# Kernel optimization log

Measured on AMD Instinct MI355X. Metric: run time of the kernel, lower is better.

The kernel has to match this reference:

```python
import jax, jax.numpy as jnp
import numpy as np

B, NO, Q = 128, 36, 14          # batch, num object regions, question length
VD, QD, H = 2048, 1024, 2048    # v_dim, q_dim, FCNet hidden dim


def setup_inputs() -> dict:
    key = jax.random.key(0)
    ks = jax.random.split(key, 10)
    s = lambda fan_in: 1.0 / np.sqrt(fan_in)
    return {
        "v": jax.random.normal(ks[0], (B, NO, VD), dtype=jnp.float32),
        "q": jax.random.normal(ks[1], (B, Q, QD), dtype=jnp.float32),
        # v_net: weight_norm Linear(v_dim, 2048) + ReLU (effective weight)
        "Wv": jax.random.normal(ks[2], (H, VD), dtype=jnp.float32) * s(VD),
        "bv": jax.random.normal(ks[3], (H,), dtype=jnp.float32) * 0.01,
        # q_net: weight_norm Linear(q_dim, 2048) + ReLU
        "Wq": jax.random.normal(ks[4], (H, QD), dtype=jnp.float32) * s(QD),
        "bq": jax.random.normal(ks[5], (H,), dtype=jnp.float32) * 0.01,
        # h_net: Linear(14, 1) applied along the question axis of d_
        "wh": jax.random.normal(ks[6], (Q,), dtype=jnp.float32) * s(Q),
        "bh": jax.random.normal(ks[7], (), dtype=jnp.float32) * 0.01,
        # h_net2: Linear(v_dim, v_dim) == Linear(2048, 2048)
        "W2": jax.random.normal(ks[8], (VD, H), dtype=jnp.float32) * s(H),
        "b2": jax.random.normal(ks[9], (VD,), dtype=jnp.float32) * 0.01,
    }


def reference(v, q, Wv, bv, Wq, bq, wh, bh, W2, b2):
    # FCNet (eval mode: dropout = identity): ReLU(weight-norm Linear)
    v_ = jax.nn.relu(jnp.einsum("bnd,hd->bnh", v, Wv) + bv)  # [B, NO, H]
    q_ = jax.nn.relu(jnp.einsum("bqd,hd->bqh", q, Wq) + bq)  # [B, Q,  H]
    # Original: d_[b,h,n,q] = v_[b,n,h] * q_[b,q,h]; logits = h_net(d_)
    # => logits[b,h,n] = sum_q v_[b,n,h] * q_[b,q,h] * wh[q] + bh
    # Fused: reduce q_ against wh first, avoiding the [B,H,NO,Q] intermediate.
    qw = jnp.einsum("bqh,q->bh", q_, wh)                     # [B, H]
    logits = v_ * qw[:, None, :] + bh                        # [B, NO, H]
    # h_net2 on last dim
    return jnp.einsum("bnh,vh->bnv", logits, W2) + b2        # [B, NO, VD]
```

## Files before the change

kernel.cpp:

```cpp
#include <hip/hip_runtime.h>
#include <hip/hip_bf16.h>


typedef __attribute__((ext_vector_type(4))) float f32x4;
typedef __attribute__((ext_vector_type(8))) short short8;

__device__ __forceinline__ short f2bf(float f) {
    union { float f; unsigned u; } x; x.f = f;
    unsigned u = x.u;
    unsigned r = (u + 0x7FFFu + ((u >> 16) & 1u)) >> 16;
    return (short)(r & 0xFFFFu);
}
__device__ __forceinline__ float bf2f(short s) {
    union { unsigned u; float f; } x; x.u = ((unsigned)(unsigned short)s) << 16;
    return x.f;
}

__device__ __forceinline__ void gload_lds16(const short* g, short* l) {
    __builtin_amdgcn_global_load_lds(
        (const __attribute__((address_space(1))) unsigned int*)g,
        (__attribute__((address_space(3))) unsigned int*)l,
        16, 0, 0);
}

#define CV0 1179648
#define CV1 1703936
#define CV2 2228224
#define CV3 2457600
#define CV4 2719744
__global__ __launch_bounds__(256)
void cvt_all(const float* __restrict__ v,  short* __restrict__ vb,
             const float* __restrict__ Wv, short* __restrict__ Wvb,
             const float* __restrict__ W2, short* __restrict__ W2b,
             const float* __restrict__ q,  short* __restrict__ qb,
             const float* __restrict__ Wq, short* __restrict__ Wqb)
{
    const int stride = gridDim.x * 256;
    for (int c = blockIdx.x * 256 + threadIdx.x; c < CV4; c += stride) {
        const float* src; short* dst; int i;
        if      (c < CV0) { src = v;  dst = vb;  i = c * 8; }
        else if (c < CV1) { src = Wv; dst = Wvb; i = (c - CV0) * 8; }
        else if (c < CV2) { src = W2; dst = W2b; i = (c - CV1) * 8; }
        else if (c < CV3) { src = q;  dst = qb;  i = (c - CV2) * 8; }
        else              { src = Wq; dst = Wqb; i = (c - CV3) * 8; }
        f32x4 a = *(const f32x4*)&src[i];
        f32x4 b = *(const f32x4*)&src[i + 4];
        short8 s;
        #pragma unroll
        for (int j = 0; j < 4; ++j) { s[j] = f2bf(a[j]); s[4 + j] = f2bf(b[j]); }
        *(short8*)&dst[i] = s;
    }
}

__global__ __launch_bounds__(256)
void gemm_bt128(const short* __restrict__ Ab, const short* __restrict__ Bb,
                const float* __restrict__ bias, void* __restrict__ Cp,
                int M, int N, int K)
{
    __shared__ short ldsA[128 * 64];
    __shared__ short ldsB[128 * 64];

    const int tid    = threadIdx.x;
    const int lane   = tid & 63;
    const int wid    = tid >> 6;
    const int wr     = wid >> 1;
    const int wc     = wid & 1;
    const int lrow   = lane & 15;
    const int lchunk = lane >> 4;

    const int row0 = blockIdx.x * 128;
    const int col0 = blockIdx.y * 128;

    const int s_r = lane >> 3;
    const int s_c = ((lane & 7) ^ s_r) * 8;

    f32x4 acc[4][4];
    #pragma unroll
    for (int i = 0; i < 4; ++i)
        #pragma unroll
        for (int j = 0; j < 4; ++j)
            acc[i][j] = (f32x4)0.0f;

    const int nk = K >> 6;

    for (int kt = 0; kt < nk; ++kt) {
        const int kc = kt * 64;
        if (kt) __syncthreads();
        #pragma unroll
        for (int i = 0; i < 4; ++i) {
            const int r = wid * 32 + i * 8 + s_r;
            gload_lds16(&Ab[(size_t)(row0 + r) * K + kc + s_c],
                        &ldsA[(wid * 32 + i * 8) * 64]);
            gload_lds16(&Bb[(size_t)(col0 + r) * K + kc + s_c],
                        &ldsB[(wid * 32 + i * 8) * 64]);
        }
        __syncthreads();

        short8 af[4][2], bfv[4][2];
        #pragma unroll
        for (int mi = 0; mi < 4; ++mi) {
            const int row = wr * 64 + mi * 16 + lrow;
            #pragma unroll
            for (int ks = 0; ks < 2; ++ks)
                af[mi][ks] = *(const short8*)((const char*)ldsA +
                    row * 128 + (((ks * 4 + lchunk) * 16) ^ ((row & 7) << 4)));
        }
        #pragma unroll
        for (int ni = 0; ni < 4; ++ni) {
            const int row = wc * 64 + ni * 16 + lrow;
            #pragma unroll
            for (int ks = 0; ks < 2; ++ks)
                bfv[ni][ks] = *(const short8*)((const char*)ldsB +
                    row * 128 + (((ks * 4 + lchunk) * 16) ^ ((row & 7) << 4)));
        }
        #pragma unroll
        for (int ks = 0; ks < 2; ++ks)
            #pragma unroll
            for (int mi = 0; mi < 4; ++mi)
                #pragma unroll
                for (int ni = 0; ni < 4; ++ni)
                    acc[mi][ni] = __builtin_amdgcn_mfma_f32_16x16x32_bf16(
                        af[mi][ks], bfv[ni][ks], acc[mi][ni], 0, 0, 0);
    }

    #pragma unroll
    for (int mi = 0; mi < 4; ++mi)
        #pragma unroll
        for (int ni = 0; ni < 4; ++ni)
            #pragma unroll
            for (int r = 0; r < 4; ++r) {
                const int row = row0 + wr * 64 + mi * 16 + lchunk * 4 + r;
                const int col = col0 + wc * 64 + ni * 16 + lrow;
                float val = fmaxf(acc[mi][ni][r] + bias[col], 0.0f);
                ((short*)Cp)[(size_t)row * N + col] = f2bf(val);
            }
}

template<int EPI>
__global__ __launch_bounds__(512, 2)
void gemm256(const short* __restrict__ Ab, const short* __restrict__ Bb,
             const float* __restrict__ bias, const float* __restrict__ qw,
             const float* __restrict__ bh_p, void* __restrict__ Cp,
             int M, int N, int K)
{
    __shared__ short lds[2][4][128 * 64];

    const int tid  = threadIdx.x;
    const int lane = tid & 63;
    const int w    = tid >> 6;
    const int wr   = w >> 2;
    const int wc   = w & 3;
    const int fr   = lane & 15;
    const int fc   = lane >> 4;

    const int row0 = blockIdx.x * 256;
    const int col0 = blockIdx.y * 256;

    const int sl_s = lane >> 3;
    const int sl_c = ((lane & 7) ^ sl_s) * 8;

    const int nt = K >> 6;

    f32x4 acc[8][4];
    #pragma unroll
    for (int i = 0; i < 8; ++i)
        #pragma unroll
        for (int j = 0; j < 4; ++j)
            acc[i][j] = (f32x4)0.0f;

    auto stageA = [&](int t, int q) {
        #pragma unroll
        for (int i = 0; i < 2; ++i) {
            const int g  = w * 2 + i;
            const int rl = g * 8 + sl_s;
            const int srow = row0 + (g >> 3) * 128 + q * 64 + (rl & 63);
            gload_lds16(&Ab[(size_t)srow * K + t * 64 + sl_c],
                        &lds[t & 1][q][g * 512]);
        }
    };
    auto stageB = [&](int t, int q) {
        #pragma unroll
        for (int i = 0; i < 2; ++i) {
            const int g  = w * 2 + i;
            const int rl = g * 8 + sl_s;
            const int srow = col0 + (rl >> 5) * 64 + q * 32 + (rl & 31);
            gload_lds16(&Bb[(size_t)srow * K + t * 64 + sl_c],
                        &lds[t & 1][2 + q][g * 512]);
        }
    };

    short8 A0[4][2], A1[4][2], B0[2][2], B1[2][2];

#define READA(T, MQ, DST)                                                       \
    _Pragma("unroll") for (int m_ = 0; m_ < 4; ++m_) {                          \
        const int rl_ = wr * 64 + m_ * 16 + fr;                                 \
        _Pragma("unroll") for (int k_ = 0; k_ < 2; ++k_)                        \
            DST[m_][k_] = *(const short8*)((const char*)&lds[(T) & 1][MQ][0]    \
                + rl_ * 128 + ((k_ * 64 + fc * 16) ^ ((rl_ & 7) << 4)));        \
    }
#define READB(T, NQ, DST)                                                       \
    _Pragma("unroll") for (int n_ = 0; n_ < 2; ++n_) {                          \
        const int rl_ = wc * 32 + n_ * 16 + fr;                                 \
        _Pragma("unroll") for (int k_ = 0; k_ < 2; ++k_)                        \
            DST[n_][k_] = *(const short8*)((const char*)&lds[(T) & 1][2 + (NQ)][0] \
                + rl_ * 128 + ((k_ * 64 + fc * 16) ^ ((rl_ & 7) << 4)));        \
    }
#define MFMAQ(MQ, NQ, ASET, BSET)                                               \
    _Pragma("unroll") for (int m_ = 0; m_ < 4; ++m_)                            \
      _Pragma("unroll") for (int n_ = 0; n_ < 2; ++n_)                          \
        _Pragma("unroll") for (int k_ = 0; k_ < 2; ++k_)                        \
          acc[(MQ) * 4 + m_][(NQ) * 2 + n_] =                                   \
              __builtin_amdgcn_mfma_f32_16x16x32_bf16(                          \
                  ASET[m_][k_], BSET[n_][k_], acc[(MQ) * 4 + m_][(NQ) * 2 + n_], 0, 0, 0);

#define BAR()   asm volatile("s_barrier" ::: "memory")
#define PRIO1() __builtin_amdgcn_s_setprio(1)
#define PRIO0() __builtin_amdgcn_s_setprio(0)
#define VM4()   asm volatile("s_waitcnt vmcnt(4)" ::: "memory")
#define VM0()   asm volatile("s_waitcnt vmcnt(0)" ::: "memory")

#define KITER(T0, T1, ST1, ST2, ST3, ST4, ST5, ST6, ST7, ST8, D4, D8)           \
  {                                                                             \
          \
    READA(T0, 0, A0); READB(T0, 0, B0);                                         \
    PRIO1(); MFMAQ(0, 0, A0, B0); PRIO0();                                      \
    READB(T0, 1, B1); ST1; BAR();                                               \
                                     \
    PRIO1(); MFMAQ(0, 1, A0, B1); PRIO0();                                      \
    READA(T0, 1, A1); ST2; BAR();                                               \
                                                      \
    PRIO1(); MFMAQ(1, 1, A1, B1); PRIO0();                                      \
    ST3; BAR();                                                                 \
                                            \
    PRIO1(); MFMAQ(1, 0, A1, B0); PRIO0();                                      \
    ST4; D4; BAR();                                                             \
          \
    READA(T1, 0, A0); READB(T1, 0, B0);                                         \
    PRIO1(); MFMAQ(0, 0, A0, B0); PRIO0();                                      \
    READB(T1, 1, B1); ST5; BAR();                                               \
                                           \
    PRIO1(); MFMAQ(0, 1, A0, B1); PRIO0();                                      \
    READA(T1, 1, A1); ST6; BAR();                                               \
                                                            \
    PRIO1(); MFMAQ(1, 1, A1, B1); PRIO0();                                      \
    ST7; BAR();                                                                 \
                                                \
    PRIO1(); MFMAQ(1, 0, A1, B0); PRIO0();                                      \
    ST8; D8; BAR();                                                             \
  }

    stageA(0, 0); stageB(0, 0); stageB(0, 1); stageA(0, 1);
    stageA(1, 0); stageB(1, 1);
    VM4();
    BAR();

    const int niter = (nt >> 1) - 1;
    for (int j = 0; j < niter; ++j) {
        const int t0 = 2 * j, t1 = 2 * j + 1;
        KITER(t0, t1,
              stageA(t1, 1),     stageB(t1, 0),
              stageA(t0 + 2, 0), stageB(t0 + 2, 1),
              stageA(t0 + 2, 1), stageB(t0 + 2, 0),
              stageA(t1 + 2, 0), stageB(t1 + 2, 1),
              VM4(), VM4());
    }
    {
        const int t0 = nt - 2, t1 = nt - 1;
        KITER(t0, t1,
              stageA(t1, 1), stageB(t1, 0),
              (void)0, (void)0, (void)0, (void)0, (void)0, (void)0,
              VM0(), (void)0);
    }

#undef KITER
#undef READA
#undef READB
#undef MFMAQ
#undef BAR
#undef PRIO1
#undef PRIO0
#undef VM4
#undef VM0

    const float bhv = (EPI == 1) ? bh_p[0] : 0.0f;
    #pragma unroll
    for (int m = 0; m < 8; ++m) {
        #pragma unroll
        for (int n = 0; n < 4; ++n) {
            #pragma unroll
            for (int r = 0; r < 4; ++r) {
                const int row = row0 + wr * 128 + m * 16 + fc * 4 + r;
                const int col = col0 + wc * 64 + n * 16 + fr;
                float val = acc[m][n][r];
                if (EPI == 1) {
                    val = fmaxf(val + bias[col], 0.0f);
                    const int b = row / 36;
                    val = val * qw[b * 2048 + col] + bhv;
                    ((short*)Cp)[(size_t)row * N + col] = f2bf(val);
                } else {
                    ((float*)Cp)[(size_t)row * N + col] = val + bias[col];
                }
            }
        }
    }
}

__global__ __launch_bounds__(256)
void qw_reduce(const short* __restrict__ q_, const float* __restrict__ wh,
               float* __restrict__ qw)
{
    const int idx = blockIdx.x * 256 + threadIdx.x;
    const int b = idx >> 11;
    const int h = idx & 2047;
    float s = 0.0f;
    #pragma unroll
    for (int qq = 0; qq < 14; ++qq)
        s += bf2f(q_[(size_t)(b * 14 + qq) * 2048 + h]) * wh[qq];
    qw[idx] = s;
}

extern "C" void kernel_launch(void* const* d_in, const int* in_sizes, int n_in,
                              void* d_out, int out_size, void* d_ws, size_t ws_size,
                              hipStream_t stream)
{
    const float* v  = (const float*)d_in[0];
    const float* q  = (const float*)d_in[1];
    const float* Wv = (const float*)d_in[2];
    const float* bv = (const float*)d_in[3];
    const float* Wq = (const float*)d_in[4];
    const float* bq = (const float*)d_in[5];
    const float* wh = (const float*)d_in[6];
    const float* bh = (const float*)d_in[7];
    const float* W2 = (const float*)d_in[8];
    const float* b2 = (const float*)d_in[9];
    float* out = (float*)d_out;

    char* ws = (char*)d_ws;
    short* vb     = (short*)(ws);
    short* Wvb    = (short*)(ws + 18874368);
    short* W2b    = (short*)(ws + 27262976);
    short* qb     = (short*)(ws + 35651584);
    short* Wqb    = (short*)(ws + 39321600);
    short* q_ws   = (short*)(ws + 43515904);
    float* qw     = (float*)(ws + 50855936);
    short* logits = (short*)(ws + 51904512);

    cvt_all<<<2048, 256, 0, stream>>>(v, vb, Wv, Wvb, W2, W2b, q, qb, Wq, Wqb);

    gemm_bt128<<<dim3(1792 / 128, 2048 / 128), 256, 0, stream>>>(
        qb, Wqb, bq, q_ws, 1792, 2048, 1024);

    qw_reduce<<<(128 * 2048) / 256, 256, 0, stream>>>(q_ws, wh, qw);

    gemm256<1><<<dim3(4608 / 256, 2048 / 256), 512, 0, stream>>>(
        vb, Wvb, bv, qw, bh, logits, 4608, 2048, 2048);

    gemm256<2><<<dim3(4608 / 256, 2048 / 256), 512, 0, stream>>>(
        logits, W2b, b2, nullptr, nullptr, out, 4608, 2048, 2048);
}
```

Measured before the change: 147.5 us.

## Overlap v/Wv/W2 bf16 conversion with the q-projection GEMM in one launch

Splits the conversion kernel so only q and Wq are converted first. The v, Wv and W2 conversion now runs in extra blocks of the q-net GEMM launch (224 GEMM blocks plus 288 conversion blocks), so the memory-bound conversion overlaps the small GEMM instead of running before it. The risk is that the two kinds of work compete for bandwidth and CU slots, and the GEMM grid is now linearized with hardcoded sizes.

```diff
diff --git a/kernel.cpp b/kernel.cpp
--- a/kernel.cpp
+++ b/kernel.cpp
@@ -23,43 +23,56 @@
         16, 0, 0);
 }
 
-#define CV0 1179648
-#define CV1 1703936
-#define CV2 2228224
-#define CV3 2457600
-#define CV4 2719744
+__device__ __forceinline__ void cvt_chunk(const float* __restrict__ src,
+                                          short* __restrict__ dst, int i)
+{
+    f32x4 a = *(const f32x4*)&src[i];
+    f32x4 b = *(const f32x4*)&src[i + 4];
+    short8 s;
+    #pragma unroll
+    for (int j = 0; j < 4; ++j) { s[j] = f2bf(a[j]); s[4 + j] = f2bf(b[j]); }
+    *(short8*)&dst[i] = s;
+}
+
+#define Q_CH  229376
+#define QW_CH 262144
 __global__ __launch_bounds__(256)
-void cvt_all(const float* __restrict__ v,  short* __restrict__ vb,
-             const float* __restrict__ Wv, short* __restrict__ Wvb,
-             const float* __restrict__ W2, short* __restrict__ W2b,
-             const float* __restrict__ q,  short* __restrict__ qb,
-             const float* __restrict__ Wq, short* __restrict__ Wqb)
-{
+void cvt_qw(const float* __restrict__ q,  short* __restrict__ qb,
+            const float* __restrict__ Wq, short* __restrict__ Wqb)
+{
+    const int total = Q_CH + QW_CH;
     const int stride = gridDim.x * 256;
-    for (int c = blockIdx.x * 256 + threadIdx.x; c < CV4; c += stride) {
-        const float* src; short* dst; int i;
-        if      (c < CV0) { src = v;  dst = vb;  i = c * 8; }
-        else if (c < CV1) { src = Wv; dst = Wvb; i = (c - CV0) * 8; }
-        else if (c < CV2) { src = W2; dst = W2b; i = (c - CV1) * 8; }
-        else if (c < CV3) { src = q;  dst = qb;  i = (c - CV2) * 8; }
-        else              { src = Wq; dst = Wqb; i = (c - CV3) * 8; }
-        f32x4 a = *(const f32x4*)&src[i];
-        f32x4 b = *(const f32x4*)&src[i + 4];
-        short8 s;
-        #pragma unroll
-        for (int j = 0; j < 4; ++j) { s[j] = f2bf(a[j]); s[4 + j] = f2bf(b[j]); }
-        *(short8*)&dst[i] = s;
-    }
-}
-
+    for (int c = blockIdx.x * 256 + threadIdx.x; c < total; c += stride) {
+        if (c < Q_CH) cvt_chunk(q, qb, c * 8);
+        else          cvt_chunk(Wq, Wqb, (c - Q_CH) * 8);
+    }
+}
+
+#define V_CH  1179648
+#define WV_CH 524288
+#define W2_CH 524288
 __global__ __launch_bounds__(256)
-void gemm_bt128(const short* __restrict__ Ab, const short* __restrict__ Bb,
-                const float* __restrict__ bias, void* __restrict__ Cp,
-                int M, int N, int K)
+void k1_fused(const short* __restrict__ Ab, const short* __restrict__ Bb,
+              const float* __restrict__ bias, short* __restrict__ Cp,
+              const float* __restrict__ v,  short* __restrict__ vb,
+              const float* __restrict__ Wv, short* __restrict__ Wvb,
+              const float* __restrict__ W2, short* __restrict__ W2b)
 {
     __shared__ short ldsA[128 * 64];
     __shared__ short ldsB[128 * 64];
 
+    if (blockIdx.x >= 224) {
+        const int total = V_CH + WV_CH + W2_CH;
+        const int stride = 288 * 256;
+        for (int c = (blockIdx.x - 224) * 256 + threadIdx.x; c < total; c += stride) {
+            if      (c < V_CH)         cvt_chunk(v,  vb,  c * 8);
+            else if (c < V_CH + WV_CH) cvt_chunk(Wv, Wvb, (c - V_CH) * 8);
+            else                       cvt_chunk(W2, W2b, (c - V_CH - WV_CH) * 8);
+        }
+        return;
+    }
+
+    const int K = 1024, N = 2048;
     const int tid    = threadIdx.x;
     const int lane   = tid & 63;
     const int wid    = tid >> 6;
@@ -68,8 +81,8 @@
     const int lrow   = lane & 15;
     const int lchunk = lane >> 4;
 
-    const int row0 = blockIdx.x * 128;
-    const int col0 = blockIdx.y * 128;
+    const int row0 = (blockIdx.x % 14) * 128;
+    const int col0 = (blockIdx.x / 14) * 128;
 
     const int s_r = lane >> 3;
     const int s_c = ((lane & 7) ^ s_r) * 8;
@@ -132,7 +145,7 @@
                 const int row = row0 + wr * 64 + mi * 16 + lchunk * 4 + r;
                 const int col = col0 + wc * 64 + ni * 16 + lrow;
                 float val = fmaxf(acc[mi][ni][r] + bias[col], 0.0f);
-                ((short*)Cp)[(size_t)row * N + col] = f2bf(val);
+                Cp[(size_t)row * N + col] = f2bf(val);
             }
 }
 
@@ -221,30 +234,22 @@
 
 #define KITER(T0, T1, ST1, ST2, ST3, ST4, ST5, ST6, ST7, ST8, D4, D8)           \
   {                                                                             \
-          \
     READA(T0, 0, A0); READB(T0, 0, B0);                                         \
     PRIO1(); MFMAQ(0, 0, A0, B0); PRIO0();                                      \
     READB(T0, 1, B1); ST1; BAR();                                               \
-                                     \
     PRIO1(); MFMAQ(0, 1, A0, B1); PRIO0();                                      \
     READA(T0, 1, A1); ST2; BAR();                                               \
-                                                      \
     PRIO1(); MFMAQ(1, 1, A1, B1); PRIO0();                                      \
     ST3; BAR();                                                                 \
-                                            \
     PRIO1(); MFMAQ(1, 0, A1, B0); PRIO0();                                      \
     ST4; D4; BAR();                                                             \
-          \
     READA(T1, 0, A0); READB(T1, 0, B0);                                         \
     PRIO1(); MFMAQ(0, 0, A0, B0); PRIO0();                                      \
     READB(T1, 1, B1); ST5; BAR();                                               \
-                                           \
     PRIO1(); MFMAQ(0, 1, A0, B1); PRIO0();                                      \
     READA(T1, 1, A1); ST6; BAR();                                               \
-                                                            \
     PRIO1(); MFMAQ(1, 1, A1, B1); PRIO0();                                      \
     ST7; BAR();                                                                 \
-                                                \
     PRIO1(); MFMAQ(1, 0, A1, B0); PRIO0();                                      \
     ST8; D8; BAR();                                                             \
   }
@@ -345,10 +350,10 @@
     float* qw     = (float*)(ws + 50855936);
     short* logits = (short*)(ws + 51904512);
 
-    cvt_all<<<2048, 256, 0, stream>>>(v, vb, Wv, Wvb, W2, W2b, q, qb, Wq, Wqb);
-
-    gemm_bt128<<<dim3(1792 / 128, 2048 / 128), 256, 0, stream>>>(
-        qb, Wqb, bq, q_ws, 1792, 2048, 1024);
+    cvt_qw<<<1024, 256, 0, stream>>>(q, qb, Wq, Wqb);
+
+    k1_fused<<<512, 256, 0, stream>>>(qb, Wqb, bq, q_ws,
+                                      v, vb, Wv, Wvb, W2, W2b);
 
     qw_reduce<<<(128 * 2048) / 256, 256, 0, stream>>>(q_ws, wh, qw);
 
```

After: 140.7 us. -4.6%, faster.
